# Performance work log

Hardware: AMD Instinct MI355X
Metric: run time of the kernel (lower is better)

Reference implementation:

```python
import jax, jax.numpy as jnp
import numpy as np

BATCH, SEQ_LEN, VEC_DIM, WIDTH = 64, 256, 512, 3


def setup_inputs() -> dict:
    key = jax.random.key(0)
    k = jax.random.split(key, 8)
    F0r = jax.random.normal(k[0], (BATCH, SEQ_LEN, VEC_DIM), jnp.float32)
    F1r = jax.random.normal(k[1], (BATCH, SEQ_LEN, VEC_DIM), jnp.float32)
    sent0_mask = (jax.random.uniform(k[2], (BATCH, SEQ_LEN)) < 0.9).astype(jnp.float32)
    sent1_mask = (jax.random.uniform(k[3], (BATCH, SEQ_LEN)) < 0.9).astype(jnp.float32)
    # nn.Parameter(torch.randn(seq_len, vec_dim))
    W0 = jax.random.normal(k[4], (SEQ_LEN, VEC_DIM), jnp.float32)
    W1 = jax.random.normal(k[5], (SEQ_LEN, VEC_DIM), jnp.float32)
    # Conv2d(2, 1, kernel_size=(WIDTH, 1)) default init: U(-1/sqrt(fan_in), +)
    bound = 1.0 / np.sqrt(2 * WIDTH * 1)
    conv_w = jax.random.uniform(k[6], (1, 2, WIDTH, 1), jnp.float32, -bound, bound)
    conv_b = jax.random.uniform(k[7], (1,), jnp.float32, -bound, bound)
    return dict(F0r=F0r, F1r=F1r, sent0_mask=sent0_mask, sent1_mask=sent1_mask,
                W0=W0, W1=W1, conv_w=conv_w, conv_b=conv_b)


def _conv_tanh_pool(x, conv_w, conv_b):
    # x: [B, 2, S, D]; conv pad (WIDTH-1, 0) -> [B, 1, S+WIDTH-1, D]
    y = jax.lax.conv_general_dilated(
        x, conv_w, window_strides=(1, 1),
        padding=((WIDTH - 1, WIDTH - 1), (0, 0)),
        dimension_numbers=('NCHW', 'OIHW', 'NCHW'))
    y = jnp.tanh(y + conv_b[None, :, None, None])
    # AvgPool2d kernel (WIDTH,1), stride 1 -> [B, 1, S, D]
    y = jax.lax.reduce_window(y, 0.0, jax.lax.add,
                              (1, 1, WIDTH, 1), (1, 1, 1, 1), 'VALID') / WIDTH
    return y[:, 0]  # squeeze channel -> [B, S, D]


def reference(F0r, F1r, sent0_mask, sent1_mask, W0, W1, conv_w, conv_b):
    # masking is in-place in the torch code, so masked F0/F1 feed the conv too
    F0 = F0r * sent0_mask[:, :, None]  # [B, S, D]
    F1 = F1r * sent1_mask[:, :, None]
    # pairwise L2 via ||u-v||^2 = ||u||^2 + ||v||^2 - 2 u.v (avoids [B,S,S,D])
    sq0 = jnp.sum(F0 * F0, axis=-1)  # [B, S]
    sq1 = jnp.sum(F1 * F1, axis=-1)
    cross = jnp.einsum('bid,bjd->bij', F0, F1)  # [B, S, S]
    d2 = jnp.maximum(sq0[:, :, None] + sq1[:, None, :] - 2.0 * cross, 0.0)
    norm = jnp.where(d2 > 0, jnp.sqrt(jnp.where(d2 > 0, d2, 1.0)), 0.0)
    A = 1.0 / (1.0 + norm)  # [B, S, S]
    F0a = jnp.einsum('bij,id->bjd', A, W0)  # A^T @ W0
    F1a = jnp.einsum('bij,jd->bid', A, W1)  # A @ W1
    x0 = jnp.stack([F0, F0a], axis=1)  # [B, 2, S, D]
    x1 = jnp.stack([F1, F1a], axis=1)
    out0 = _conv_tanh_pool(x0, conv_w, conv_b)
    out1 = _conv_tanh_pool(x1, conv_w, conv_b)
    return out0, out1
```

## Files before the change

### kernel.cpp

```cpp
#include <hip/hip_runtime.h>

typedef unsigned short u16;
typedef __attribute__((ext_vector_type(8))) short short8;
typedef __attribute__((ext_vector_type(4))) float f32x4;

__device__ inline u16 f2bf(float f) {
    union { float f; unsigned u; } v; v.f = f;
    unsigned u = v.u;
    unsigned r = (u + 0x7FFFu + ((u >> 16) & 1u)) >> 16;
    return (u16)r;
}
__device__ inline float bf2f(u16 h) {
    union { unsigned u; float f; } v; v.u = ((unsigned)h) << 16;
    return v.f;
}
__device__ inline float ftanh(float x) {
    float e = __expf(2.f * x);
    return 1.f - 2.f / (e + 1.f);
}
__device__ inline float4 bf4f(ushort4 u) {
    float4 f; f.x = bf2f(u.x); f.y = bf2f(u.y); f.z = bf2f(u.z); f.w = bf2f(u.w);
    return f;
}

__global__ __launch_bounds__(128) void prep_kernel(
    const float* __restrict__ F0r, const float* __restrict__ F1r,
    const float* __restrict__ m0, const float* __restrict__ m1,
    const float* __restrict__ W0, const float* __restrict__ W1,
    u16* __restrict__ F0b, u16* __restrict__ F1b,
    u16* __restrict__ WT0, u16* __restrict__ WT1,
    float* __restrict__ sq0, float* __restrict__ sq1)
{
    int bx = blockIdx.x;
    int t = threadIdx.x;
    if (bx >= 16384) {
        int idx = (bx - 16384) * 128 + t;
        int a = idx >> 17;
        int r = idx & 131071;
        int s = r >> 9, d = r & 511;
        const float* W = a ? W1 : W0;
        u16* WT = a ? WT1 : WT0;
        WT[d * 256 + s] = f2bf(W[r]);
        return;
    }
    int bs = bx;
    size_t base = (size_t)bs * 512 + t * 4;
    float mk0 = m0[bs], mk1 = m1[bs];
    float4 v0 = *(const float4*)(F0r + base);
    float4 v1 = *(const float4*)(F1r + base);
    v0.x *= mk0; v0.y *= mk0; v0.z *= mk0; v0.w *= mk0;
    v1.x *= mk1; v1.y *= mk1; v1.z *= mk1; v1.w *= mk1;
    ushort4 u0; u0.x = f2bf(v0.x); u0.y = f2bf(v0.y); u0.z = f2bf(v0.z); u0.w = f2bf(v0.w);
    ushort4 u1; u1.x = f2bf(v1.x); u1.y = f2bf(v1.y); u1.z = f2bf(v1.z); u1.w = f2bf(v1.w);
    *(ushort4*)(F0b + base) = u0;
    *(ushort4*)(F1b + base) = u1;
    float s0p = v0.x*v0.x + v0.y*v0.y + v0.z*v0.z + v0.w*v0.w;
    float s1p = v1.x*v1.x + v1.y*v1.y + v1.z*v1.z + v1.w*v1.w;
    #pragma unroll
    for (int off = 32; off > 0; off >>= 1) {
        s0p += __shfl_xor(s0p, off);
        s1p += __shfl_xor(s1p, off);
    }
    __shared__ float red0[2], red1[2];
    if ((t & 63) == 0) { red0[t >> 6] = s0p; red1[t >> 6] = s1p; }
    __syncthreads();
    if (t == 0) { sq0[bs] = red0[0] + red0[1]; sq1[bs] = red1[0] + red1[1]; }
}

__global__ __launch_bounds__(256) void gemm_cross_kernel(
    const u16* __restrict__ F0b, const u16* __restrict__ F1b,
    const float* __restrict__ sq0, const float* __restrict__ sq1,
    u16* __restrict__ Abf, u16* __restrict__ ATbf)
{
    __shared__ __align__(16) u16 smem[64 * 136 * 2];
    u16 (*As)[136] = (u16(*)[136])smem;
    u16 (*Bs)[136] = (u16(*)[136])(smem + 64 * 136);

    int b = blockIdx.y;
    int i0 = (blockIdx.x >> 2) * 64, j0 = (blockIdx.x & 3) * 64;
    const u16* Ap = F0b + (size_t)b * 131072;
    const u16* Bp = F1b + (size_t)b * 131072;
    const float* sqR = sq0 + b * 256;
    const float* sqC = sq1 + b * 256;

    const int t = threadIdx.x;
    const int lane = t & 63, w = t >> 6;
    const int wm = w >> 1, wn = w & 1;
    const int q = lane >> 4, lm = lane & 15;

    f32x4 acc[2][2];
    #pragma unroll
    for (int x = 0; x < 2; ++x)
        #pragma unroll
        for (int y = 0; y < 2; ++y)
            acc[x][y] = (f32x4){0.f, 0.f, 0.f, 0.f};

    for (int k0 = 0; k0 < 512; k0 += 128) {
        #pragma unroll
        for (int i = 0; i < 4; ++i) {
            int idx = i * 256 + t;
            int row = idx >> 4;
            int seg = idx & 15;
            *(uint4*)&As[row][seg * 8] =
                *(const uint4*)(Ap + (size_t)(i0 + row) * 512 + k0 + seg * 8);
            *(uint4*)&Bs[row][seg * 8] =
                *(const uint4*)(Bp + (size_t)(j0 + row) * 512 + k0 + seg * 8);
        }
        __syncthreads();
        #pragma unroll
        for (int ks = 0; ks < 128; ks += 32) {
            short8 af[2], bfr[2];
            #pragma unroll
            for (int x = 0; x < 2; ++x) {
                af[x]  = *(const short8*)&As[wm * 32 + x * 16 + lm][ks + q * 8];
                bfr[x] = *(const short8*)&Bs[wn * 32 + x * 16 + lm][ks + q * 8];
            }
            #pragma unroll
            for (int x = 0; x < 2; ++x)
                #pragma unroll
                for (int y = 0; y < 2; ++y)
                    acc[x][y] = __builtin_amdgcn_mfma_f32_16x16x32_bf16(
                        af[x], bfr[y], acc[x][y], 0, 0, 0);
        }
        __syncthreads();
    }

    u16 (*Ct)[136] = (u16(*)[136])smem;
    #pragma unroll
    for (int x = 0; x < 2; ++x) {
        #pragma unroll
        for (int r = 0; r < 4; ++r) {
            int ir = wm * 32 + x * 16 + q * 4 + r;
            float si = sqR[i0 + ir];
            #pragma unroll
            for (int y = 0; y < 2; ++y) {
                int jc = wn * 32 + y * 16 + lm;
                float d2 = si + sqC[j0 + jc] - 2.f * acc[x][y][r];
                d2 = fmaxf(d2, 0.f);
                float a = 1.f / (1.f + sqrtf(d2));
                Ct[ir][jc] = f2bf(a);
            }
        }
    }
    __syncthreads();

    u16* Aout  = Abf  + (size_t)b * 65536;
    u16* ATout = ATbf + (size_t)b * 65536;
    int ii = t >> 2;
    int c0 = (t & 3) * 16;
    #pragma unroll
    for (int c = 0; c < 4; ++c) {
        ushort4 v = *(ushort4*)&Ct[ii][c0 + c * 4];
        *(ushort4*)&Aout[(size_t)(i0 + ii) * 256 + j0 + c0 + c * 4] = v;
    }
    #pragma unroll
    for (int c = 0; c < 4; ++c) {
        ushort4 v;
        v.x = Ct[c0 + c * 4 + 0][ii];
        v.y = Ct[c0 + c * 4 + 1][ii];
        v.z = Ct[c0 + c * 4 + 2][ii];
        v.w = Ct[c0 + c * 4 + 3][ii];
        *(ushort4*)&ATout[(size_t)(j0 + ii) * 256 + i0 + c0 + c * 4] = v;
    }
}

__global__ __launch_bounds__(256) void fa_conv_kernel(
    const u16* __restrict__ Abf, const u16* __restrict__ ATbf,
    const u16* __restrict__ WT0, const u16* __restrict__ WT1,
    const u16* __restrict__ F0b, const u16* __restrict__ F1b,
    const float* __restrict__ cw, const float* __restrict__ cb,
    float* __restrict__ out)
{
    __shared__ __align__(16) u16 Al[36][264];
    __shared__ __align__(16) u16 BlFl[128 * 72];
    u16 (*Bl)[72]  = (u16(*)[72])BlFl;
    u16 (*Fl)[132] = (u16(*)[132])BlFl;

    int b = blockIdx.y, side = blockIdx.z;
    int s0 = blockIdx.x * 32;
    const u16* Ap = (side ? Abf : ATbf) + (size_t)b * 65536;
    const u16* WT = side ? WT1 : WT0;
    const u16* Fb = (side ? F1b : F0b) + (size_t)b * 131072;
    float* o = out + (size_t)side * 8388608 + (size_t)b * 131072;

    const int t = threadIdx.x;
    const int lane = t & 63, w = t >> 6;
    const int q = lane >> 4, lm = lane & 15;

    #pragma unroll
    for (int i = 0; i < 5; ++i) {
        int idx = i * 256 + t;
        if (idx < 1152) {
            int r = idx >> 5;
            int seg = idx & 31;
            int s = s0 - 2 + r;
            uint4 v = {0u, 0u, 0u, 0u};
            if ((unsigned)s < 256u)
                v = *(const uint4*)(Ap + (size_t)s * 256 + seg * 8);
            *(uint4*)&Al[r][seg * 8] = v;
        }
    }

    const u16* aRow[3];
    aRow[0] = &Al[lm][0];
    aRow[1] = &Al[16 + lm][0];
    aRow[2] = &Al[(lm < 4) ? (32 + lm) : 0][0];

    float w00 = cw[0], w01 = cw[1], w02 = cw[2];
    float w10 = cw[3], w11 = cw[4], w12 = cw[5];
    float bias = cb[0];
    const float third = 1.f / 3.f;
    const int g = t >> 5;
    const int dl = (t & 31) * 4;

    for (int n0 = 0; n0 < 512; n0 += 128) {
        f32x4 acc[3][2];
        #pragma unroll
        for (int x = 0; x < 3; ++x)
            #pragma unroll
            for (int y = 0; y < 2; ++y)
                acc[x][y] = (f32x4){0.f, 0.f, 0.f, 0.f};

        for (int kb = 0; kb < 256; kb += 64) {
            __syncthreads();
            #pragma unroll
            for (int i = 0; i < 4; ++i) {
                int idx = i * 256 + t;
                int r = idx >> 3;
                int seg = idx & 7;
                *(uint4*)&Bl[r][seg * 8] =
                    *(const uint4*)(WT + (size_t)(n0 + r) * 256 + kb + seg * 8);
            }
            __syncthreads();
            #pragma unroll
            for (int ks = 0; ks < 64; ks += 32) {
                short8 af[3], bfr[2];
                #pragma unroll
                for (int x = 0; x < 3; ++x)
                    af[x] = *(const short8*)(aRow[x] + kb + ks + q * 8);
                #pragma unroll
                for (int y = 0; y < 2; ++y)
                    bfr[y] = *(const short8*)&Bl[w * 32 + y * 16 + lm][ks + q * 8];
                #pragma unroll
                for (int x = 0; x < 3; ++x)
                    #pragma unroll
                    for (int y = 0; y < 2; ++y)
                        acc[x][y] = __builtin_amdgcn_mfma_f32_16x16x32_bf16(
                            af[x], bfr[y], acc[x][y], 0, 0, 0);
            }
        }
        __syncthreads();

        #pragma unroll
        for (int x = 0; x < 3; ++x)
            #pragma unroll
            for (int r = 0; r < 4; ++r) {
                int m = x * 16 + q * 4 + r;
                if (m < 36) {
                    #pragma unroll
                    for (int y = 0; y < 2; ++y)
                        Fl[m][w * 32 + y * 16 + lm] = f2bf(acc[x][y][r]);
                }
            }
        __syncthreads();

        float4 f[8], a[8];
        #pragma unroll
        for (int k = 0; k < 8; ++k) {
            int s = s0 + g * 4 - 2 + k;
            if ((unsigned)s < 256u)
                f[k] = bf4f(*(const ushort4*)(Fb + (size_t)s * 512 + n0 + dl));
            else
                f[k] = make_float4(0.f, 0.f, 0.f, 0.f);
            a[k] = bf4f(*(const ushort4*)&Fl[g * 4 + k][dl]);
        }
        float4 ty[6];
        #pragma unroll
        for (int k = 0; k < 6; ++k) {
            float4 y;
            y.x = bias + w00*f[k].x + w01*f[k+1].x + w02*f[k+2].x + w10*a[k].x + w11*a[k+1].x + w12*a[k+2].x;
            y.y = bias + w00*f[k].y + w01*f[k+1].y + w02*f[k+2].y + w10*a[k].y + w11*a[k+1].y + w12*a[k+2].y;
            y.z = bias + w00*f[k].z + w01*f[k+1].z + w02*f[k+2].z + w10*a[k].z + w11*a[k+1].z + w12*a[k+2].z;
            y.w = bias + w00*f[k].w + w01*f[k+1].w + w02*f[k+2].w + w10*a[k].w + w11*a[k+1].w + w12*a[k+2].w;
            y.x = ftanh(y.x); y.y = ftanh(y.y); y.z = ftanh(y.z); y.w = ftanh(y.w);
            ty[k] = y;
        }
        #pragma unroll
        for (int r = 0; r < 4; ++r) {
            float4 res;
            res.x = (ty[r].x + ty[r+1].x + ty[r+2].x) * third;
            res.y = (ty[r].y + ty[r+1].y + ty[r+2].y) * third;
            res.z = (ty[r].z + ty[r+1].z + ty[r+2].z) * third;
            res.w = (ty[r].w + ty[r+1].w + ty[r+2].w) * third;
            *(float4*)(o + (size_t)(s0 + g * 4 + r) * 512 + n0 + dl) = res;
        }
    }
}

extern "C" void kernel_launch(void* const* d_in, const int* in_sizes, int n_in,
                              void* d_out, int out_size, void* d_ws, size_t ws_size,
                              hipStream_t stream)
{
    const float* F0r = (const float*)d_in[0];
    const float* F1r = (const float*)d_in[1];
    const float* m0  = (const float*)d_in[2];
    const float* m1  = (const float*)d_in[3];
    const float* W0  = (const float*)d_in[4];
    const float* W1  = (const float*)d_in[5];
    const float* cw  = (const float*)d_in[6];
    const float* cb  = (const float*)d_in[7];
    float* out = (float*)d_out;

    char* ws = (char*)d_ws;
    u16* F0b   = (u16*)(ws);
    u16* F1b   = (u16*)(ws + 16777216);
    u16* Abf   = (u16*)(ws + 33554432);
    u16* ATbf  = (u16*)(ws + 41943040);
    float* sq0 = (float*)(ws + 50331648);
    float* sq1 = (float*)(ws + 50397184);
    u16* WT0   = (u16*)(ws + 50462720);
    u16* WT1   = (u16*)(ws + 50724864);

    prep_kernel<<<18432, 128, 0, stream>>>(F0r, F1r, m0, m1, W0, W1,
                                           F0b, F1b, WT0, WT1, sq0, sq1);
    gemm_cross_kernel<<<dim3(16, 64), 256, 0, stream>>>(F0b, F1b, sq0, sq1, Abf, ATbf);
    fa_conv_kernel<<<dim3(8, 64, 2), 256, 0, stream>>>(Abf, ATbf, WT0, WT1,
                                                       F0b, F1b, cw, cb, out);
}
```

Before: 203.6 us.

## Double-buffer GEMM tiles via direct global-to-LDS loads with XOR swizzle

Both MFMA kernels now stage operand tiles with global_load_lds (direct global-to-LDS DMA) into double buffers, prefetching the next K chunk while computing the current one. This removes one barrier per iteration and hides global load latency. An XOR swizzle replaces row padding to avoid LDS bank conflicts. In fa_conv the next n0 block's first B tile is prefetched during the conv epilogue. The cost is more shared memory, which may lower occupancy. Correctness depends on the implicit wave-based LDS destination layout matching the swizzled reads.

```diff
diff --git a/kernel.cpp b/kernel.cpp
--- a/kernel.cpp
+++ b/kernel.cpp
@@ -21,6 +21,12 @@
 __device__ inline float4 bf4f(ushort4 u) {
     float4 f; f.x = bf2f(u.x); f.y = bf2f(u.y); f.z = bf2f(u.z); f.w = bf2f(u.w);
     return f;
+}
+
+typedef const __attribute__((address_space(1))) void* gas_ptr;
+typedef __attribute__((address_space(3))) void* las_ptr;
+__device__ __forceinline__ void gl2lds16(const u16* g, u16* l) {
+    __builtin_amdgcn_global_load_lds((gas_ptr)(const void*)g, (las_ptr)(void*)l, 16, 0, 0);
 }
 
 __global__ __launch_bounds__(128) void prep_kernel(
@@ -72,9 +78,7 @@
     const float* __restrict__ sq0, const float* __restrict__ sq1,
     u16* __restrict__ Abf, u16* __restrict__ ATbf)
 {
-    __shared__ __align__(16) u16 smem[64 * 136 * 2];
-    u16 (*As)[136] = (u16(*)[136])smem;
-    u16 (*Bs)[136] = (u16(*)[136])(smem + 64 * 136);
+    __shared__ __align__(16) u16 smem[4 * 8192];
 
     int b = blockIdx.y;
     int i0 = (blockIdx.x >> 2) * 64, j0 = (blockIdx.x & 3) * 64;
@@ -88,6 +92,19 @@
     const int wm = w >> 1, wn = w & 1;
     const int q = lane >> 4, lm = lane & 15;
 
+#define STAGE_AB(bufo, k0) do {                                                \
+    _Pragma("unroll")                                                          \
+    for (int i_ = 0; i_ < 4; ++i_) {                                           \
+        int idx_ = i_ * 256 + t;                                               \
+        int row_ = idx_ >> 4, seg_ = idx_ & 15;                                \
+        int ss_  = seg_ ^ (row_ & 7);                                          \
+        int lo_  = (bufo) + (i_ * 256 + w * 64) * 8;         \
+        gl2lds16(Ap + (size_t)(i0 + row_) * 512 + (k0) + ss_ * 8,              \
+                 &smem[lo_]);                                                  \
+        gl2lds16(Bp + (size_t)(j0 + row_) * 512 + (k0) + ss_ * 8,              \
+                 &smem[lo_ + 8192]);                                           \
+    } } while (0)
+
     f32x4 acc[2][2];
     #pragma unroll
     for (int x = 0; x < 2; ++x)
@@ -95,25 +112,24 @@
         for (int y = 0; y < 2; ++y)
             acc[x][y] = (f32x4){0.f, 0.f, 0.f, 0.f};
 
-    for (int k0 = 0; k0 < 512; k0 += 128) {
-        #pragma unroll
-        for (int i = 0; i < 4; ++i) {
-            int idx = i * 256 + t;
-            int row = idx >> 4;
-            int seg = idx & 15;
-            *(uint4*)&As[row][seg * 8] =
-                *(const uint4*)(Ap + (size_t)(i0 + row) * 512 + k0 + seg * 8);
-            *(uint4*)&Bs[row][seg * 8] =
-                *(const uint4*)(Bp + (size_t)(j0 + row) * 512 + k0 + seg * 8);
-        }
+    STAGE_AB(0, 0);
+
+    #pragma unroll
+    for (int c = 0; c < 4; ++c) {
         __syncthreads();
+        if (c < 3)
+            STAGE_AB(((c + 1) & 1) * 16384, (c + 1) * 128);
+        const int cb = (c & 1) * 16384;
         #pragma unroll
         for (int ks = 0; ks < 128; ks += 32) {
             short8 af[2], bfr[2];
             #pragma unroll
             for (int x = 0; x < 2; ++x) {
-                af[x]  = *(const short8*)&As[wm * 32 + x * 16 + lm][ks + q * 8];
-                bfr[x] = *(const short8*)&Bs[wn * 32 + x * 16 + lm][ks + q * 8];
+                int ra = wm * 32 + x * 16 + lm;
+                int rb = wn * 32 + x * 16 + lm;
+                int su = (((ks >> 3) + q) ^ (lm & 7)) * 8;
+                af[x]  = *(const short8*)&smem[cb + ra * 128 + su];
+                bfr[x] = *(const short8*)&smem[cb + 8192 + rb * 128 + su];
             }
             #pragma unroll
             for (int x = 0; x < 2; ++x)
@@ -122,8 +138,9 @@
                     acc[x][y] = __builtin_amdgcn_mfma_f32_16x16x32_bf16(
                         af[x], bfr[y], acc[x][y], 0, 0, 0);
         }
-        __syncthreads();
-    }
+    }
+    __syncthreads();
+#undef STAGE_AB
 
     u16 (*Ct)[136] = (u16(*)[136])smem;
     #pragma unroll
@@ -172,9 +189,8 @@
     float* __restrict__ out)
 {
     __shared__ __align__(16) u16 Al[36][264];
-    __shared__ __align__(16) u16 BlFl[128 * 72];
-    u16 (*Bl)[72]  = (u16(*)[72])BlFl;
-    u16 (*Fl)[132] = (u16(*)[132])BlFl;
+    __shared__ __align__(16) u16 BlBuf[2 * 8192];
+    __shared__ __align__(16) u16 Fl[36][132];
 
     int b = blockIdx.y, side = blockIdx.z;
     int s0 = blockIdx.x * 32;
@@ -186,6 +202,16 @@
     const int t = threadIdx.x;
     const int lane = t & 63, w = t >> 6;
     const int q = lane >> 4, lm = lane & 15;
+
+#define STAGE_B(bufo, nn, kb) do {                                             \
+    _Pragma("unroll")                                                          \
+    for (int i_ = 0; i_ < 4; ++i_) {                                           \
+        int idx_ = i_ * 256 + t;                                               \
+        int r_ = idx_ >> 3, seg_ = idx_ & 7;                                   \
+        int ss_ = seg_ ^ (r_ & 7);                                             \
+        gl2lds16(WT + (size_t)((nn) + r_) * 256 + (kb) + ss_ * 8,              \
+                 &BlBuf[(bufo) + (i_ * 256 + w * 64) * 8]);                    \
+    } } while (0)
 
     #pragma unroll
     for (int i = 0; i < 5; ++i) {
@@ -213,6 +239,8 @@
     const int g = t >> 5;
     const int dl = (t & 31) * 4;
 
+    STAGE_B(0, 0, 0);
+
     for (int n0 = 0; n0 < 512; n0 += 128) {
         f32x4 acc[3][2];
         #pragma unroll
@@ -221,17 +249,13 @@
             for (int y = 0; y < 2; ++y)
                 acc[x][y] = (f32x4){0.f, 0.f, 0.f, 0.f};
 
-        for (int kb = 0; kb < 256; kb += 64) {
+        #pragma unroll
+        for (int kb_i = 0; kb_i < 4; ++kb_i) {
             __syncthreads();
-            #pragma unroll
-            for (int i = 0; i < 4; ++i) {
-                int idx = i * 256 + t;
-                int r = idx >> 3;
-                int seg = idx & 7;
-                *(uint4*)&Bl[r][seg * 8] =
-                    *(const uint4*)(WT + (size_t)(n0 + r) * 256 + kb + seg * 8);
-            }
-            __syncthreads();
+            if (kb_i < 3)
+                STAGE_B(((kb_i + 1) & 1) * 8192, n0, (kb_i + 1) * 64);
+            const int cbuf = (kb_i & 1) * 8192;
+            const int kb = kb_i * 64;
             #pragma unroll
             for (int ks = 0; ks < 64; ks += 32) {
                 short8 af[3], bfr[2];
@@ -239,8 +263,11 @@
                 for (int x = 0; x < 3; ++x)
                     af[x] = *(const short8*)(aRow[x] + kb + ks + q * 8);
                 #pragma unroll
-                for (int y = 0; y < 2; ++y)
-                    bfr[y] = *(const short8*)&Bl[w * 32 + y * 16 + lm][ks + q * 8];
+                for (int y = 0; y < 2; ++y) {
+                    int rb = w * 32 + y * 16 + lm;
+                    int su = (((ks >> 3) + q) ^ (lm & 7)) * 8;
+                    bfr[y] = *(const short8*)&BlBuf[cbuf + rb * 64 + su];
+                }
                 #pragma unroll
                 for (int x = 0; x < 3; ++x)
                     #pragma unroll
@@ -249,7 +276,6 @@
                             af[x], bfr[y], acc[x][y], 0, 0, 0);
             }
         }
-        __syncthreads();
 
         #pragma unroll
         for (int x = 0; x < 3; ++x)
@@ -264,6 +290,9 @@
             }
         __syncthreads();
 
+        if (n0 < 384)
+            STAGE_B(0, n0 + 128, 0);
+
         float4 f[8], a[8];
         #pragma unroll
         for (int k = 0; k < 8; ++k) {
@@ -295,6 +324,7 @@
             *(float4*)(o + (size_t)(s0 + g * 4 + r) * 512 + n0 + dl) = res;
         }
     }
+#undef STAGE_B
 }
 
 extern "C" void kernel_launch(void* const* d_in, const int* in_sizes, int n_in,
```

After: 201.4 us. About the same (-1.1%).
